# Optimization experiments

Hardware: AMD Instinct MI355X
Metric: run time of the kernel (lower is better)

The kernel has to match this reference:

```python
import jax, jax.numpy as jnp
import numpy as np

B = 2048   # batch size
D = 2048   # feature dim (ResNet-50)
H = 2048   # projection hidden dim
T = 0.1    # temperature
EPS_BN = 1e-5
CC_ITERS = 32  # >= ~2*log2(B), enough for pointer-jumping convergence


def setup_inputs() -> dict:
    key = jax.random.key(0)
    ks = jax.random.split(key, 4)
    s = 0.02
    return {
        "x1": jax.random.normal(ks[0], (B, D), dtype=jnp.float32),
        "x2": jax.random.normal(ks[1], (B, D), dtype=jnp.float32),
        "W1": jax.random.normal(ks[2], (H, D), dtype=jnp.float32) * s,
        "b1": jnp.zeros((H,), jnp.float32),
        "gamma": jnp.ones((H,), jnp.float32),
        "beta": jnp.zeros((H,), jnp.float32),
        "W2": jax.random.normal(ks[3], (D, H), dtype=jnp.float32) * s,
        "b2": jnp.zeros((D,), jnp.float32),
    }


def _head(x, W1, b1, gamma, beta, W2, b2):
    # ProjectionHead: Linear -> BatchNorm1d (train mode, batch stats) -> ReLU -> Linear
    h = x @ W1.T + b1
    mu = h.mean(0)
    var = h.var(0)  # biased variance, as torch BN uses for normalization
    h = (h - mu) * jax.lax.rsqrt(var + EPS_BN) * gamma + beta
    h = jax.nn.relu(h)
    o = h @ W2.T + b2
    n = jnp.maximum(jnp.linalg.norm(o, axis=1, keepdims=True), 1e-12)
    return o / n  # F.normalize


def _cc_mask(feat):
    # build_connected_component: kNN(k=1) graph + connected components -> same-label mask
    b = feat.shape[0]
    sim = jax.lax.stop_gradient(feat @ feat.T) - 2.0 * jnp.eye(b, dtype=feat.dtype)
    y = jnp.argmax(sim, axis=1)  # topk(1) neighbor per row
    # min-label propagation with pointer jumping (GPU-native union-find equivalent)
    def body(_, l):
        ln = jnp.minimum(l, l[y])      # propagate along edge i -> y[i]
        ln = ln.at[y].min(l)           # propagate along reverse edge y[i] -> i
        return jnp.minimum(ln, ln[ln])  # pointer jumping
    labels = jax.lax.fori_loop(0, CC_ITERS, body, jnp.arange(b))
    return (labels[:, None] == labels[None, :]).astype(feat.dtype)


def _sup_contra(logits, mask, diag):
    dm = 1.0 - diag
    mask = mask * dm
    exp_logits = jnp.exp(logits) * dm
    log_prob = logits - jnp.log(exp_logits.sum(1, keepdims=True))
    mean_log_prob_pos = (mask * log_prob).sum(1) / mask.sum(1)
    return (-mean_log_prob_pos).mean()


def reference(x1, x2, W1, b1, gamma, beta, W2, b2):
    # Only head2 branch contributes to the returned graph_loss (head1 branch is dead code
    # w.r.t. the return value), so we compute exactly the graph_loss path.
    feat1 = _head(x1, W1, b1, gamma, beta, W2, b2)
    feat2 = _head(x2, W1, b1, gamma, beta, W2, b2)
    mask1 = _cc_mask(feat1)
    mask2 = _cc_mask(feat2)
    diag = jnp.eye(B, dtype=feat1.dtype)
    loss = _sup_contra(feat1 @ feat1.T / T, mask2, diag)
    loss = loss + _sup_contra(feat2 @ feat2.T / T, mask1, diag)
    return loss / 2.0
```

## Files before the change

kernel.cpp:

```cpp
#include <hip/hip_runtime.h>
#include <hip/hip_bf16.h>

typedef __bf16 bf16_t;
typedef __bf16 bf16x4 __attribute__((ext_vector_type(4)));
typedef __bf16 bf16x8 __attribute__((ext_vector_type(8)));
typedef float  f32x4  __attribute__((ext_vector_type(4)));

__device__ __forceinline__ void gload_lds16(const void* g, void* l)
{
    __builtin_amdgcn_global_load_lds((__attribute__((address_space(1))) void*)g,
                                     (__attribute__((address_space(3))) void*)l,
                                     16, 0, 0);
}

__global__ __launch_bounds__(256) void cast_all(const float* __restrict__ x1, const float* __restrict__ x2,
                                                const float* __restrict__ W1, const float* __restrict__ W2,
                                                bf16_t* __restrict__ xcatb, bf16_t* __restrict__ W1b,
                                                bf16_t* __restrict__ W2b)
{
    const size_t i  = ((size_t)blockIdx.x * 256 + threadIdx.x) * 4;
    const size_t M4 = 1ull << 22;
    const size_t r  = i >> 22;
    const size_t off = i & (M4 - 1);
    const float* src; bf16_t* dst;
    if (r == 0)      { src = x1; dst = xcatb; }
    else if (r == 1) { src = x2; dst = xcatb + M4; }
    else if (r == 2) { src = W1; dst = W1b; }
    else             { src = W2; dst = W2b; }
    f32x4 v = *(const f32x4*)(src + off);
    bf16x4 o;
    o[0] = (bf16_t)v[0]; o[1] = (bf16_t)v[1]; o[2] = (bf16_t)v[2]; o[3] = (bf16_t)v[3];
    *(bf16x4*)(dst + off) = o;
}

__global__ __launch_bounds__(512, 1) void gemm8b(
    const bf16_t* __restrict__ A, const bf16_t* __restrict__ B,
    const float* __restrict__ bias, bf16_t* __restrict__ C,
    long long b_batch_stride, int mode,
    float* __restrict__ ps, float* __restrict__ ps2,
    float* __restrict__ rsq, const float* __restrict__ rnv,
    unsigned long long* __restrict__ pkey, float* __restrict__ lseP)
{
    __shared__ bf16_t lsA[4][256 * 32];
    __shared__ bf16_t lsB[4][128 * 32];
    __shared__ float  cs2[8][64], cq2[8][64];
    __shared__ float  rq2[8][64];
    __shared__ float  ls2[8][64];
    __shared__ unsigned long long kv2[8][64];
    const int tid  = threadIdx.x;
    const int lane = tid & 63;
    const int wave = tid >> 6;
    const int l15  = lane & 15;
    const int cg   = lane >> 4;
    const int wm   = (wave >> 1) * 64;
    const int wn   = (wave & 1) * 64;
    const int m0   = blockIdx.y * 256;
    const int n0   = blockIdx.x * 128;
    const int K = 2048, N = 2048, NT = 32;
    const bf16_t* Bb = B + (size_t)(m0 >> 11) * b_batch_stride;

    f32x4 acc[4][4] = {};

    auto STAGE_A = [&](int k0, bf16_t* dst) {
#pragma unroll
        for (int i = 0; i < 2; ++i) {
            const int ch  = wave * 128 + i * 64 + lane;
            const int row = ch >> 2;
            const int cs  = ((ch & 3) - ((row >> 1) & 3)) & 3;
            gload_lds16(A + (size_t)(m0 + row) * K + k0 + cs * 8, dst + ch * 8);
        }
    };
    auto STAGE_B = [&](int k0, bf16_t* dst) {
        const int ch  = wave * 64 + lane;
        const int row = ch >> 2;
        const int cs  = ((ch & 3) - ((row >> 1) & 3)) & 3;
        gload_lds16(Bb + (size_t)(n0 + row) * K + k0 + cs * 8, dst + ch * 8);
    };
    auto FRAG = [&](const bf16_t* u, int row) -> bf16x8 {
        const int p = (cg + (row >> 1)) & 3;
        return *(const bf16x8*)&u[row * 32 + p * 8];
    };

    STAGE_A(0,  lsA[0]); STAGE_B(0,  lsB[0]);
    STAGE_A(32, lsA[1]); STAGE_B(32, lsB[1]);
    asm volatile("s_waitcnt vmcnt(3)" ::: "memory");
    __builtin_amdgcn_sched_barrier(0);
    __builtin_amdgcn_s_barrier();

    for (int t = 0; t < NT; ++t) {
        const int s0 = (2 * t) & 3, s1 = (2 * t + 1) & 3;
        const int s2 = (2 * t + 2) & 3, s3 = (2 * t + 3) & 3;
        const bool st = (t < NT - 1);
        const int kn = (t + 1) * 64;
        bf16x8 af[4], bfr[4];

#pragma unroll
        for (int f = 0; f < 4; ++f) af[f]  = FRAG(lsA[s0], wm + f * 16 + l15);
#pragma unroll
        for (int f = 0; f < 4; ++f) bfr[f] = FRAG(lsB[s0], wn + f * 16 + l15);
        if (st) { STAGE_A(kn, lsA[s2]); STAGE_B(kn, lsB[s2]);
                  asm volatile("s_waitcnt vmcnt(3)" ::: "memory"); }
        else      asm volatile("s_waitcnt vmcnt(0)" ::: "memory");
        __builtin_amdgcn_sched_barrier(0);
        __builtin_amdgcn_s_barrier();
        __builtin_amdgcn_sched_barrier(0);
        __builtin_amdgcn_s_setprio(1);
#pragma unroll
        for (int fm = 0; fm < 4; ++fm)
#pragma unroll
            for (int fn = 0; fn < 4; ++fn)
                acc[fm][fn] = __builtin_amdgcn_mfma_f32_16x16x32_bf16(af[fm], bfr[fn], acc[fm][fn], 0, 0, 0);
        __builtin_amdgcn_s_setprio(0);
        __builtin_amdgcn_sched_barrier(0);
        __builtin_amdgcn_s_barrier();

#pragma unroll
        for (int f = 0; f < 4; ++f) af[f]  = FRAG(lsA[s1], wm + f * 16 + l15);
#pragma unroll
        for (int f = 0; f < 4; ++f) bfr[f] = FRAG(lsB[s1], wn + f * 16 + l15);
        if (st) { STAGE_A(kn + 32, lsA[s3]); STAGE_B(kn + 32, lsB[s3]);
                  asm volatile("s_waitcnt vmcnt(3)" ::: "memory"); }
        __builtin_amdgcn_sched_barrier(0);
        __builtin_amdgcn_s_barrier();
        __builtin_amdgcn_sched_barrier(0);
        __builtin_amdgcn_s_setprio(1);
#pragma unroll
        for (int fm = 0; fm < 4; ++fm)
#pragma unroll
            for (int fn = 0; fn < 4; ++fn)
                acc[fm][fn] = __builtin_amdgcn_mfma_f32_16x16x32_bf16(af[fm], bfr[fn], acc[fm][fn], 0, 0, 0);
        __builtin_amdgcn_s_setprio(0);
        __builtin_amdgcn_sched_barrier(0);
        __builtin_amdgcn_s_barrier();
    }

    if (mode == 2) {
        const int rnb = (m0 >> 11) * 2048;
#pragma unroll
        for (int fm = 0; fm < 4; ++fm) {
            const int mb = m0 + wm + fm * 16 + cg * 4;
            const f32x4 rm = *(const f32x4*)&rnv[mb];
#pragma unroll
            for (int fn = 0; fn < 4; ++fn) {
                const float rc = rnv[rnb + n0 + wn + fn * 16 + l15];
#pragma unroll
                for (int r = 0; r < 4; ++r)
                    acc[fm][fn][r] *= rm[r] * rc;
            }
        }
    }

#pragma unroll
    for (int fm = 0; fm < 4; ++fm) {
        const int rb = m0 + wm + fm * 16 + cg * 4;
#pragma unroll
        for (int fn = 0; fn < 4; ++fn) {
            const int colg = n0 + wn + fn * 16 + l15;
            const float bv = bias ? bias[colg] : 0.0f;
#pragma unroll
            for (int r = 0; r < 4; ++r)
                C[(size_t)(rb + r) * N + colg] = (bf16_t)(acc[fm][fn][r] + bv);
        }
    }

    if (mode == 1) {
#pragma unroll
        for (int fn = 0; fn < 4; ++fn) {
            const int cl = fn * 16 + l15;
            const float bv = bias[n0 + wn + cl];
            float s = 0.f, q = 0.f;
#pragma unroll
            for (int fm = 0; fm < 4; ++fm)
#pragma unroll
                for (int r = 0; r < 4; ++r) {
                    const float v = acc[fm][fn][r] + bv;
                    s += v; q += v * v;
                }
            s += __shfl_xor(s, 16); q += __shfl_xor(q, 16);
            s += __shfl_xor(s, 32); q += __shfl_xor(q, 32);
            if (lane < 16) { cs2[wave][cl] = s; cq2[wave][cl] = q; }
        }
        __syncthreads();
        if (tid < 128) {
            const int p = tid >> 6, cl = tid & 63;
            ps [(size_t)blockIdx.y * 2048 + n0 + tid] =
                cs2[p][cl] + cs2[p + 2][cl] + cs2[p + 4][cl] + cs2[p + 6][cl];
            ps2[(size_t)blockIdx.y * 2048 + n0 + tid] =
                cq2[p][cl] + cq2[p + 2][cl] + cq2[p + 4][cl] + cq2[p + 6][cl];
        }
    } else if (mode == 3) {
#pragma unroll
        for (int fm = 0; fm < 4; ++fm)
#pragma unroll
            for (int r = 0; r < 4; ++r) {
                float q = 0.f;
#pragma unroll
                for (int fn = 0; fn < 4; ++fn) {
                    const float v = acc[fm][fn][r] + bias[n0 + wn + fn * 16 + l15];
                    q += v * v;
                }
                q += __shfl_xor(q, 1); q += __shfl_xor(q, 2);
                q += __shfl_xor(q, 4); q += __shfl_xor(q, 8);
                if (l15 == 0) rq2[wave][fm * 16 + cg * 4 + r] = q;
            }
        __syncthreads();
        if (tid < 256) {
            const int mg = tid >> 6, rl = tid & 63;
            rsq[(size_t)blockIdx.x * 4096 + m0 + tid] = rq2[2 * mg][rl] + rq2[2 * mg + 1][rl];
        }
    } else if (mode == 2) {
#pragma unroll
        for (int fm = 0; fm < 4; ++fm)
#pragma unroll
            for (int r = 0; r < 4; ++r) {
                const int rl   = fm * 16 + cg * 4 + r;
                const int self = (m0 + wm + rl) & 2047;
                float best = -1.0e38f; int bi = 0x7fffffff; float se = 0.f;
#pragma unroll
                for (int fn = 0; fn < 4; ++fn) {
                    const int cgl = n0 + wn + fn * 16 + l15;
                    const float v = acc[fm][fn][r];
                    if (cgl != self) {
                        se += expf(10.0f * v);
                        if (v > best) { best = v; bi = cgl; }
                    }
                }
#pragma unroll
                for (int st2 = 1; st2 <= 8; st2 <<= 1) {
                    const float ov = __shfl_xor(best, st2);
                    const int   oi = __shfl_xor(bi, st2);
                    if (ov > best || (ov == best && oi < bi)) { best = ov; bi = oi; }
                    se += __shfl_xor(se, st2);
                }
                if (l15 == 0) {
                    unsigned u = __float_as_uint(best);
                    u = (u & 0x80000000u) ? ~u : (u | 0x80000000u);
                    kv2[wave][rl] = ((unsigned long long)u << 32) | (unsigned)(~bi);
                    ls2[wave][rl] = se;
                }
            }
        __syncthreads();
        if (tid < 256) {
            const int mg = tid >> 6, rl = tid & 63;
            const unsigned long long a = kv2[2 * mg][rl], b = kv2[2 * mg + 1][rl];
            pkey[(size_t)blockIdx.x * 4096 + m0 + tid] = a > b ? a : b;
            lseP[(size_t)blockIdx.x * 4096 + m0 + tid] = ls2[2 * mg][rl] + ls2[2 * mg + 1][rl];
        }
    }
}

__global__ __launch_bounds__(256) void bn_final2(const float* __restrict__ ps, const float* __restrict__ ps2,
                                                 float* __restrict__ mu, float* __restrict__ rinv)
{
    const int c = blockIdx.x * 256 + threadIdx.x;
    const int b = c >> 11, col = c & 2047;
    float s = 0.f, s2 = 0.f;
    for (int i = 0; i < 8; ++i) {
        s  += ps [(size_t)(b * 8 + i) * 2048 + col];
        s2 += ps2[(size_t)(b * 8 + i) * 2048 + col];
    }
    const float m = s * (1.0f / 2048.0f);
    const float v = s2 * (1.0f / 2048.0f) - m * m;
    mu[c]   = m;
    rinv[c] = rsqrtf(v + 1e-5f);
}

__global__ __launch_bounds__(256) void bn_apply(const bf16_t* __restrict__ h, const float* __restrict__ mu,
                                                const float* __restrict__ rinv, const float* __restrict__ gamma,
                                                const float* __restrict__ beta, bf16_t* __restrict__ out)
{
    const size_t base = ((size_t)blockIdx.x * 256 + threadIdx.x) * 8;
    const int col = (int)(base & 2047);
    const int br  = (int)(base >> 22);
    bf16x8 v = *(const bf16x8*)(h + base);
    bf16x8 o;
#pragma unroll
    for (int j = 0; j < 8; ++j) {
        const int c = col + j;
        const float f = (float)v[j];
        const float t = (f - mu[br * 2048 + c]) * rinv[br * 2048 + c] * gamma[c] + beta[c];
        o[j] = (bf16_t)fmaxf(t, 0.0f);
    }
    *(bf16x8*)(out + base) = o;
}

__global__ __launch_bounds__(256) void norm_final(const float* __restrict__ rsq, float* __restrict__ rn)
{
    const int r = blockIdx.x * 256 + threadIdx.x;
    float s = 0.f;
    for (int nb = 0; nb < 16; ++nb) s += rsq[(size_t)nb * 4096 + r];
    rn[r] = 1.0f / fmaxf(sqrtf(s), 1e-12f);
}

__global__ __launch_bounds__(1024) void cc_labels(const unsigned long long* __restrict__ pkey,
                                                  int* __restrict__ labg)
{
    __shared__ int A_[2048];
    __shared__ int Bn[2048];
    __shared__ int Y_[2048];
    __shared__ int chg;
    const int br = blockIdx.x;
    const int t = threadIdx.x;
    if (t == 0) chg = 0;
    for (int i = t; i < 2048; i += 1024) {
        const int row = br * 2048 + i;
        unsigned long long k = 0ull;
        for (int nb = 0; nb < 16; ++nb) {
            const unsigned long long v = pkey[(size_t)nb * 4096 + row];
            k = (v > k) ? v : k;
        }
        Y_[i] = (int)~((unsigned)(k & 0xFFFFFFFFull));
        A_[i] = i;
    }
    __syncthreads();
    for (int it = 0; it < 32; ++it) {
        for (int i = t; i < 2048; i += 1024) Bn[i] = min(A_[i], A_[Y_[i]]);
        __syncthreads();
        for (int i = t; i < 2048; i += 1024) atomicMin(&Bn[Y_[i]], A_[i]);
        __syncthreads();
        int ch = 0;
        for (int i = t; i < 2048; i += 1024) {
            const int b = Bn[i];
            const int nv = min(b, Bn[b]);
            if (nv != A_[i]) { ch = 1; A_[i] = nv; }
        }
        if (ch) atomicOr(&chg, 1);
        __syncthreads();
        const int c = chg;
        __syncthreads();
        if (t == 0) chg = 0;
        if (!c) break;
    }
    for (int i = t; i < 2048; i += 1024) labg[br * 2048 + i] = A_[i];
}

__global__ __launch_bounds__(256) void loss_rows(const bf16_t* __restrict__ simb, const int* __restrict__ labels,
                                                 const float* __restrict__ lseP, float* __restrict__ terms)
{
    const int row = blockIdx.x;
    const int br  = row >> 11;
    const int* lab = labels + ((1 - br) << 11);
    const int self = row & 2047;
    const int li = lab[self];
    const int t = threadIdx.x;
    const bf16x8 v8 = *(const bf16x8*)(simb + (size_t)row * 2048 + t * 8);
    float psum = 0.f; int pc = 0;
#pragma unroll
    for (int j = 0; j < 8; ++j) {
        const int c = t * 8 + j;
        if (c == self) continue;
        if (lab[c] == li) { psum += 10.0f * (float)v8[j]; pc++; }
    }
    __shared__ float PS[256]; __shared__ int PC[256];
    PS[t] = psum; PC[t] = pc;
    __syncthreads();
    for (int off = 128; off; off >>= 1) {
        if (t < off) { PS[t] += PS[t + off]; PC[t] += PC[t + off]; }
        __syncthreads();
    }
    if (t == 0) {
        float se = 0.f;
        for (int nb = 0; nb < 16; ++nb) se += lseP[(size_t)nb * 4096 + row];
        terms[row] = logf(se) - PS[0] / (float)PC[0];
    }
}

__global__ __launch_bounds__(1024) void final_reduce(const float* __restrict__ terms, float* __restrict__ out)
{
    const int t = threadIdx.x;
    float s = terms[t] + terms[t + 1024] + terms[t + 2048] + terms[t + 3072];
    __shared__ float S[1024];
    S[t] = s;
    __syncthreads();
    for (int off = 512; off; off >>= 1) { if (t < off) S[t] += S[t + off]; __syncthreads(); }
    if (t == 0) out[0] = S[0] * (1.0f / 4096.0f);
}

extern "C" void kernel_launch(void* const* d_in, const int* in_sizes, int n_in,
                              void* d_out, int out_size, void* d_ws, size_t ws_size,
                              hipStream_t stream)
{
    const float* x1    = (const float*)d_in[0];
    const float* x2    = (const float*)d_in[1];
    const float* W1    = (const float*)d_in[2];
    const float* b1    = (const float*)d_in[3];
    const float* gamma = (const float*)d_in[4];
    const float* beta  = (const float*)d_in[5];
    const float* W2    = (const float*)d_in[6];
    const float* b2    = (const float*)d_in[7];

    char* ws = (char*)d_ws;
    const size_t MB = 1024ull * 1024ull;
    const size_t NN = 2048ull * 2048ull;
    bf16_t* W1b    = (bf16_t*)(ws + 0);
    bf16_t* W2b    = (bf16_t*)(ws + 8 * MB);
    bf16_t* xcatb  = (bf16_t*)(ws + 16 * MB);
    bf16_t* hnb    = (bf16_t*)(ws + 16 * MB);
    bf16_t* hb16   = (bf16_t*)(ws + 32 * MB);
    bf16_t* ob16   = (bf16_t*)(ws + 64 * MB);
    bf16_t* simb   = (bf16_t*)(ws + 0);
    float*  psA    = (float*)(ws + 80 * MB);
    float*  psB    = psA + 32 * 2048;
    float*  rsq    = psB + 32 * 2048;
    float*  mu     = rsq + 16 * 4096;
    float*  rinv   = mu + 4096;
    float*  rn     = rinv + 4096;
    float*  lseP   = rn + 4096;
    unsigned long long* pkey = (unsigned long long*)(lseP + 16 * 4096);
    int*    labels = (int*)(pkey + 16 * 4096);
    float*  terms  = (float*)(labels + 4096);

    cast_all<<<16384, 256, 0, stream>>>(x1, x2, W1, W2, xcatb, W1b, W2b);

    gemm8b<<<dim3(16, 16), 512, 0, stream>>>(xcatb, W1b, b1, hb16, 0, 1,
                                             psA, psB, nullptr, nullptr, nullptr, nullptr);
    bn_final2<<<16, 256, 0, stream>>>(psA, psB, mu, rinv);
    bn_apply<<<4096, 256, 0, stream>>>(hb16, mu, rinv, gamma, beta, hnb);

    gemm8b<<<dim3(16, 16), 512, 0, stream>>>(hnb, W2b, b2, ob16, 0, 3,
                                             nullptr, nullptr, rsq, nullptr, nullptr, nullptr);
    norm_final<<<16, 256, 0, stream>>>(rsq, rn);

    gemm8b<<<dim3(16, 16), 512, 0, stream>>>(ob16, ob16, nullptr, simb, (long long)NN, 2,
                                             nullptr, nullptr, nullptr, rn, pkey, lseP);

    cc_labels<<<2, 1024, 0, stream>>>(pkey, labels);
    loss_rows<<<4096, 256, 0, stream>>>(simb, labels, lseP, terms);
    final_reduce<<<1, 1024, 0, stream>>>(terms, (float*)d_out);
}
```

Measured before the change: 216.4 us.

## Rework GEMM to 4-wave blocks with 128x64 warp tiles and 3-stage LDS ring

Rewrites the GEMM kernel to use 256 threads per block, with each wave computing a 128x64 sub-tile (8x4 MFMA fragments), instead of 512 threads with 64x64 per wave. The previous four-slot double-step pipeline becomes a three-slot LDS ring buffer processed one K-step at a time, and epilogue scratch now aliases the ring memory. The aim is less LDS traffic per MFMA and the chance of two resident blocks per CU. In exchange each thread holds twice as many accumulator registers, which may limit occupancy or cause spills.

```diff
diff --git a/kernel.cpp b/kernel.cpp
--- a/kernel.cpp
+++ b/kernel.cpp
@@ -33,7 +33,7 @@
     *(bf16x4*)(dst + off) = o;
 }
 
-__global__ __launch_bounds__(512, 1) void gemm8b(
+__global__ __launch_bounds__(256, 2) void gemm8c(
     const bf16_t* __restrict__ A, const bf16_t* __restrict__ B,
     const float* __restrict__ bias, bf16_t* __restrict__ C,
     long long b_batch_stride, int mode,
@@ -41,103 +41,95 @@
     float* __restrict__ rsq, const float* __restrict__ rnv,
     unsigned long long* __restrict__ pkey, float* __restrict__ lseP)
 {
-    __shared__ bf16_t lsA[4][256 * 32];
-    __shared__ bf16_t lsB[4][128 * 32];
-    __shared__ float  cs2[8][64], cq2[8][64];
-    __shared__ float  rq2[8][64];
-    __shared__ float  ls2[8][64];
-    __shared__ unsigned long long kv2[8][64];
+    __shared__ __align__(16) char ringc[3 * 24576];
+    bf16_t* ring = (bf16_t*)ringc;
     const int tid  = threadIdx.x;
     const int lane = tid & 63;
     const int wave = tid >> 6;
     const int l15  = lane & 15;
     const int cg   = lane >> 4;
-    const int wm   = (wave >> 1) * 64;
+    const int wm   = (wave >> 1) * 128;
     const int wn   = (wave & 1) * 64;
     const int m0   = blockIdx.y * 256;
     const int n0   = blockIdx.x * 128;
-    const int K = 2048, N = 2048, NT = 32;
+    const int K = 2048, N = 2048;
     const bf16_t* Bb = B + (size_t)(m0 >> 11) * b_batch_stride;
 
-    f32x4 acc[4][4] = {};
-
-    auto STAGE_A = [&](int k0, bf16_t* dst) {
-#pragma unroll
-        for (int i = 0; i < 2; ++i) {
-            const int ch  = wave * 128 + i * 64 + lane;
-            const int row = ch >> 2;
-            const int cs  = ((ch & 3) - ((row >> 1) & 3)) & 3;
-            gload_lds16(A + (size_t)(m0 + row) * K + k0 + cs * 8, dst + ch * 8);
-        }
-    };
-    auto STAGE_B = [&](int k0, bf16_t* dst) {
-        const int ch  = wave * 64 + lane;
-        const int row = ch >> 2;
-        const int cs  = ((ch & 3) - ((row >> 1) & 3)) & 3;
-        gload_lds16(Bb + (size_t)(n0 + row) * K + k0 + cs * 8, dst + ch * 8);
+    f32x4 acc[8][4] = {};
+
+    int aro[4], acs[4], bro[2], bcs[2];
+#pragma unroll
+    for (int i = 0; i < 4; ++i) {
+        const int ch = i * 256 + tid;
+        aro[i] = ch >> 2;
+        acs[i] = ((ch & 3) - ((aro[i] >> 1) & 3)) & 3;
+    }
+#pragma unroll
+    for (int i = 0; i < 2; ++i) {
+        const int ch = i * 256 + tid;
+        bro[i] = ch >> 2;
+        bcs[i] = ((ch & 3) - ((bro[i] >> 1) & 3)) & 3;
+    }
+
+    auto STAGE = [&](int k0, int u) {
+        bf16_t* uA = ring + u * 12288;
+        bf16_t* uB = uA + 8192;
+#pragma unroll
+        for (int i = 0; i < 4; ++i)
+            gload_lds16(A + (size_t)(m0 + aro[i]) * K + k0 + acs[i] * 8,
+                        uA + (i * 256 + tid) * 8);
+#pragma unroll
+        for (int i = 0; i < 2; ++i)
+            gload_lds16(Bb + (size_t)(n0 + bro[i]) * K + k0 + bcs[i] * 8,
+                        uB + (i * 256 + tid) * 8);
     };
     auto FRAG = [&](const bf16_t* u, int row) -> bf16x8 {
         const int p = (cg + (row >> 1)) & 3;
         return *(const bf16x8*)&u[row * 32 + p * 8];
     };
 
-    STAGE_A(0,  lsA[0]); STAGE_B(0,  lsB[0]);
-    STAGE_A(32, lsA[1]); STAGE_B(32, lsB[1]);
-    asm volatile("s_waitcnt vmcnt(3)" ::: "memory");
+    STAGE(0,  0);
+    STAGE(32, 1);
+    asm volatile("s_waitcnt vmcnt(6)" ::: "memory");
     __builtin_amdgcn_sched_barrier(0);
     __builtin_amdgcn_s_barrier();
 
-    for (int t = 0; t < NT; ++t) {
-        const int s0 = (2 * t) & 3, s1 = (2 * t + 1) & 3;
-        const int s2 = (2 * t + 2) & 3, s3 = (2 * t + 3) & 3;
-        const bool st = (t < NT - 1);
-        const int kn = (t + 1) * 64;
-        bf16x8 af[4], bfr[4];
-
-#pragma unroll
-        for (int f = 0; f < 4; ++f) af[f]  = FRAG(lsA[s0], wm + f * 16 + l15);
-#pragma unroll
-        for (int f = 0; f < 4; ++f) bfr[f] = FRAG(lsB[s0], wn + f * 16 + l15);
-        if (st) { STAGE_A(kn, lsA[s2]); STAGE_B(kn, lsB[s2]);
-                  asm volatile("s_waitcnt vmcnt(3)" ::: "memory"); }
-        else      asm volatile("s_waitcnt vmcnt(0)" ::: "memory");
+    int rd = 0, stg = 2;
+    for (int p = 0; p < 64; ++p) {
+        const bf16_t* uA = ring + rd * 12288;
+        const bf16_t* uB = uA + 8192;
+        bf16x8 af[8], bfr[4];
+#pragma unroll
+        for (int f = 0; f < 8; ++f) af[f]  = FRAG(uA, wm + f * 16 + l15);
+#pragma unroll
+        for (int f = 0; f < 4; ++f) bfr[f] = FRAG(uB, wn + f * 16 + l15);
+        if (p <= 61) {
+            STAGE((p + 2) * 32, stg);
+            asm volatile("s_waitcnt vmcnt(6)" ::: "memory");
+        } else if (p == 62) {
+            asm volatile("s_waitcnt vmcnt(0)" ::: "memory");
+        }
         __builtin_amdgcn_sched_barrier(0);
         __builtin_amdgcn_s_barrier();
         __builtin_amdgcn_sched_barrier(0);
         __builtin_amdgcn_s_setprio(1);
 #pragma unroll
-        for (int fm = 0; fm < 4; ++fm)
+        for (int fm = 0; fm < 8; ++fm)
 #pragma unroll
             for (int fn = 0; fn < 4; ++fn)
                 acc[fm][fn] = __builtin_amdgcn_mfma_f32_16x16x32_bf16(af[fm], bfr[fn], acc[fm][fn], 0, 0, 0);
         __builtin_amdgcn_s_setprio(0);
         __builtin_amdgcn_sched_barrier(0);
         __builtin_amdgcn_s_barrier();
-
-#pragma unroll
-        for (int f = 0; f < 4; ++f) af[f]  = FRAG(lsA[s1], wm + f * 16 + l15);
-#pragma unroll
-        for (int f = 0; f < 4; ++f) bfr[f] = FRAG(lsB[s1], wn + f * 16 + l15);
-        if (st) { STAGE_A(kn + 32, lsA[s3]); STAGE_B(kn + 32, lsB[s3]);
-                  asm volatile("s_waitcnt vmcnt(3)" ::: "memory"); }
-        __builtin_amdgcn_sched_barrier(0);
-        __builtin_amdgcn_s_barrier();
-        __builtin_amdgcn_sched_barrier(0);
-        __builtin_amdgcn_s_setprio(1);
-#pragma unroll
-        for (int fm = 0; fm < 4; ++fm)
-#pragma unroll
-            for (int fn = 0; fn < 4; ++fn)
-                acc[fm][fn] = __builtin_amdgcn_mfma_f32_16x16x32_bf16(af[fm], bfr[fn], acc[fm][fn], 0, 0, 0);
-        __builtin_amdgcn_s_setprio(0);
-        __builtin_amdgcn_sched_barrier(0);
-        __builtin_amdgcn_s_barrier();
-    }
+        rd  = (rd  == 2) ? 0 : rd + 1;
+        stg = (stg == 2) ? 0 : stg + 1;
+    }
+    __syncthreads();
 
     if (mode == 2) {
         const int rnb = (m0 >> 11) * 2048;
 #pragma unroll
-        for (int fm = 0; fm < 4; ++fm) {
+        for (int fm = 0; fm < 8; ++fm) {
             const int mb = m0 + wm + fm * 16 + cg * 4;
             const f32x4 rm = *(const f32x4*)&rnv[mb];
 #pragma unroll
@@ -151,7 +143,7 @@
     }
 
 #pragma unroll
-    for (int fm = 0; fm < 4; ++fm) {
+    for (int fm = 0; fm < 8; ++fm) {
         const int rb = m0 + wm + fm * 16 + cg * 4;
 #pragma unroll
         for (int fn = 0; fn < 4; ++fn) {
@@ -164,13 +156,15 @@
     }
 
     if (mode == 1) {
+        float* cs2 = (float*)ringc;
+        float* cq2 = cs2 + 256;
 #pragma unroll
         for (int fn = 0; fn < 4; ++fn) {
             const int cl = fn * 16 + l15;
             const float bv = bias[n0 + wn + cl];
             float s = 0.f, q = 0.f;
 #pragma unroll
-            for (int fm = 0; fm < 4; ++fm)
+            for (int fm = 0; fm < 8; ++fm)
 #pragma unroll
                 for (int r = 0; r < 4; ++r) {
                     const float v = acc[fm][fn][r] + bv;
@@ -178,19 +172,18 @@
                 }
             s += __shfl_xor(s, 16); q += __shfl_xor(q, 16);
             s += __shfl_xor(s, 32); q += __shfl_xor(q, 32);
-            if (lane < 16) { cs2[wave][cl] = s; cq2[wave][cl] = q; }
+            if (lane < 16) { cs2[wave * 64 + cl] = s; cq2[wave * 64 + cl] = q; }
         }
         __syncthreads();
         if (tid < 128) {
-            const int p = tid >> 6, cl = tid & 63;
-            ps [(size_t)blockIdx.y * 2048 + n0 + tid] =
-                cs2[p][cl] + cs2[p + 2][cl] + cs2[p + 4][cl] + cs2[p + 6][cl];
-            ps2[(size_t)blockIdx.y * 2048 + n0 + tid] =
-                cq2[p][cl] + cq2[p + 2][cl] + cq2[p + 4][cl] + cq2[p + 6][cl];
+            const int nh = tid >> 6, cl = tid & 63;
+            ps [(size_t)blockIdx.y * 2048 + n0 + tid] = cs2[nh * 64 + cl] + cs2[(nh + 2) * 64 + cl];
+            ps2[(size_t)blockIdx.y * 2048 + n0 + tid] = cq2[nh * 64 + cl] + cq2[(nh + 2) * 64 + cl];
         }
     } else if (mode == 3) {
-#pragma unroll
-        for (int fm = 0; fm < 4; ++fm)
+        float* rq2 = (float*)ringc;
+#pragma unroll
+        for (int fm = 0; fm < 8; ++fm)
 #pragma unroll
             for (int r = 0; r < 4; ++r) {
                 float q = 0.f;
@@ -201,16 +194,18 @@
                 }
                 q += __shfl_xor(q, 1); q += __shfl_xor(q, 2);
                 q += __shfl_xor(q, 4); q += __shfl_xor(q, 8);
-                if (l15 == 0) rq2[wave][fm * 16 + cg * 4 + r] = q;
+                if (l15 == 0) rq2[wave * 128 + fm * 16 + cg * 4 + r] = q;
             }
         __syncthreads();
-        if (tid < 256) {
-            const int mg = tid >> 6, rl = tid & 63;
-            rsq[(size_t)blockIdx.x * 4096 + m0 + tid] = rq2[2 * mg][rl] + rq2[2 * mg + 1][rl];
+        {
+            const int mh = tid >> 7, rl = tid & 127;
+            rsq[(size_t)blockIdx.x * 4096 + m0 + tid] = rq2[2 * mh * 128 + rl] + rq2[(2 * mh + 1) * 128 + rl];
         }
     } else if (mode == 2) {
-#pragma unroll
-        for (int fm = 0; fm < 4; ++fm)
+        float* ls2 = (float*)ringc;
+        unsigned long long* kv2 = (unsigned long long*)(ringc + 4096);
+#pragma unroll
+        for (int fm = 0; fm < 8; ++fm)
 #pragma unroll
             for (int r = 0; r < 4; ++r) {
                 const int rl   = fm * 16 + cg * 4 + r;
@@ -235,16 +230,16 @@
                 if (l15 == 0) {
                     unsigned u = __float_as_uint(best);
                     u = (u & 0x80000000u) ? ~u : (u | 0x80000000u);
-                    kv2[wave][rl] = ((unsigned long long)u << 32) | (unsigned)(~bi);
-                    ls2[wave][rl] = se;
+                    kv2[wave * 128 + rl] = ((unsigned long long)u << 32) | (unsigned)(~bi);
+                    ls2[wave * 128 + rl] = se;
                 }
             }
         __syncthreads();
-        if (tid < 256) {
-            const int mg = tid >> 6, rl = tid & 63;
-            const unsigned long long a = kv2[2 * mg][rl], b = kv2[2 * mg + 1][rl];
+        {
+            const int mh = tid >> 7, rl = tid & 127;
+            const unsigned long long a = kv2[2 * mh * 128 + rl], b = kv2[(2 * mh + 1) * 128 + rl];
             pkey[(size_t)blockIdx.x * 4096 + m0 + tid] = a > b ? a : b;
-            lseP[(size_t)blockIdx.x * 4096 + m0 + tid] = ls2[2 * mg][rl] + ls2[2 * mg + 1][rl];
+            lseP[(size_t)blockIdx.x * 4096 + m0 + tid] = ls2[2 * mh * 128 + rl] + ls2[(2 * mh + 1) * 128 + rl];
         }
     }
 }
@@ -412,16 +407,16 @@
 
     cast_all<<<16384, 256, 0, stream>>>(x1, x2, W1, W2, xcatb, W1b, W2b);
 
-    gemm8b<<<dim3(16, 16), 512, 0, stream>>>(xcatb, W1b, b1, hb16, 0, 1,
+    gemm8c<<<dim3(16, 16), 256, 0, stream>>>(xcatb, W1b, b1, hb16, 0, 1,
                                              psA, psB, nullptr, nullptr, nullptr, nullptr);
     bn_final2<<<16, 256, 0, stream>>>(psA, psB, mu, rinv);
     bn_apply<<<4096, 256, 0, stream>>>(hb16, mu, rinv, gamma, beta, hnb);
 
-    gemm8b<<<dim3(16, 16), 512, 0, stream>>>(hnb, W2b, b2, ob16, 0, 3,
+    gemm8c<<<dim3(16, 16), 256, 0, stream>>>(hnb, W2b, b2, ob16, 0, 3,
                                              nullptr, nullptr, rsq, nullptr, nullptr, nullptr);
     norm_final<<<16, 256, 0, stream>>>(rsq, rn);
 
-    gemm8b<<<dim3(16, 16), 512, 0, stream>>>(ob16, ob16, nullptr, simb, (long long)NN, 2,
+    gemm8c<<<dim3(16, 16), 256, 0, stream>>>(ob16, ob16, nullptr, simb, (long long)NN, 2,
                                              nullptr, nullptr, nullptr, rn, pkey, lseP);
 
     cc_labels<<<2, 1024, 0, stream>>>(pkey, labels);
```

Result: slower. 235.1 us (+8.7%).
